# Optimization experiments

Measured on AMD Instinct MI355X. Metric: run time of the kernel, lower is better.

## Reference

```python
import jax, jax.numpy as jnp
import numpy as np

D_MODEL = 1024
NUM_HEADS = 16
H_DIM = 4096
EPS = 1e-5


def setup_inputs() -> dict:
    key = jax.random.key(0)
    ks = jax.random.split(key, 16)
    B, S, D, H = 2, 2048, D_MODEL, H_DIM
    s = 0.02
    return {
        "x": jax.random.normal(ks[0], (B, S, D), jnp.float32),
        "wq": jax.random.normal(ks[1], (D, D), jnp.float32) * s,
        "bq": jnp.zeros((D,), jnp.float32),
        "wk": jax.random.normal(ks[2], (D, D), jnp.float32) * s,
        "bk": jnp.zeros((D,), jnp.float32),
        "wv": jax.random.normal(ks[3], (D, D), jnp.float32) * s,
        "bv": jnp.zeros((D,), jnp.float32),
        "wo": jax.random.normal(ks[4], (D, D), jnp.float32) * s,
        "bo": jnp.zeros((D,), jnp.float32),
        "ln1_g": jnp.ones((D,), jnp.float32),
        "ln1_b": jnp.zeros((D,), jnp.float32),
        "w1": jax.random.normal(ks[5], (H, D), jnp.float32) * s,
        "b1": jnp.zeros((H,), jnp.float32),
        "w2": jax.random.normal(ks[6], (D, H), jnp.float32) * s,
        "b2": jnp.zeros((D,), jnp.float32),
        "ln2_g": jnp.ones((D,), jnp.float32),
        "ln2_b": jnp.zeros((D,), jnp.float32),
    }


def _layer_norm(x, g, b):
    mu = jnp.mean(x, axis=-1, keepdims=True)
    var = jnp.mean(jnp.square(x - mu), axis=-1, keepdims=True)
    return (x - mu) * jax.lax.rsqrt(var + EPS) * g + b


def _mhsa(x, wq, bq, wk, bk, wv, bv, wo, bo):
    B, S, D = x.shape
    Hh, hd = NUM_HEADS, D // NUM_HEADS
    q = (x @ wq.T + bq).reshape(B, S, Hh, hd)
    k = (x @ wk.T + bk).reshape(B, S, Hh, hd)
    v = (x @ wv.T + bv).reshape(B, S, Hh, hd)
    scale = hd ** -0.5
    scores = jnp.einsum('bqhd,bkhd->bhqk', q, k) * scale
    att = jax.nn.softmax(scores, axis=-1)
    out = jnp.einsum('bhqk,bkhd->bqhd', att, v).reshape(B, S, D)
    return out @ wo.T + bo


def reference(x, wq, bq, wk, bk, wv, bv, wo, bo, ln1_g, ln1_b,
              w1, b1, w2, b2, ln2_g, ln2_b):
    # pre-norm variant as written in the torch source:
    # x = norm1(x); x = x + msa(x)  (residual uses NORMALIZED x)
    x = _layer_norm(x, ln1_g, ln1_b)
    x = x + _mhsa(x, wq, bq, wk, bk, wv, bv, wo, bo)
    x = _layer_norm(x, ln2_g, ln2_b)
    h = jax.nn.gelu(x @ w1.T + b1, approximate=False)
    x = x + (h @ w2.T + b2)
    return x
```

## Files before the change

### kernel.cpp

```cpp
#include <hip/hip_runtime.h>
#include <hip/hip_bf16.h>

typedef unsigned short u16;
typedef __attribute__((ext_vector_type(8))) short short8;
typedef __attribute__((ext_vector_type(4))) float f32x4;

#define DM 1024
#define HM 4096
#define NHEADS 16
#define HD 64
#define SQ 2048
#define NBATCH 2
#define NTOK 4096

#define NX  ((size_t)NTOK * DM)

__device__ __forceinline__ u16 f2b(float f) {
    union { float f; unsigned int i; } w; w.f = f;
    unsigned int x = w.i;
    return (u16)((x + 0x7FFFu + ((x >> 16) & 1u)) >> 16);
}
__device__ __forceinline__ u16 f2b_ru(float f) {
    union { float f; unsigned int i; } w; w.f = f;
    return (u16)((w.i + 0x8000u) >> 16);
}

__device__ __forceinline__ void gload_lds16(const void* g, void* l) {
    __builtin_amdgcn_global_load_lds(
        (const __attribute__((address_space(1))) void*)g,
        (__attribute__((address_space(3))) void*)l, 16, 0, 0);
}

__global__ void cvt_all(const float* __restrict__ wq, const float* __restrict__ wk,
                        const float* __restrict__ wv, const float* __restrict__ wo,
                        const float* __restrict__ w1, const float* __restrict__ w2,
                        u16* __restrict__ dst) {
    const int NW4 = DM * DM / 4;
    int i = blockIdx.x * 256 + threadIdx.x;
    if (i >= 12 * NW4) return;
    const float* src; int base; float sc = 1.0f;
    if      (i <     NW4) { src = wq; base = 0;       sc = 0.125f; }
    else if (i < 2 * NW4) { src = wk; base = NW4; }
    else if (i < 3 * NW4) { src = wv; base = 2 * NW4; }
    else if (i < 4 * NW4) { src = wo; base = 3 * NW4; }
    else if (i < 8 * NW4) { src = w1; base = 4 * NW4; }
    else                  { src = w2; base = 8 * NW4; }
    float4 f = ((const float4*)src)[i - base];
    ushort4 o;
    o.x = f2b(f.x * sc); o.y = f2b(f.y * sc);
    o.z = f2b(f.z * sc); o.w = f2b(f.w * sc);
    ((ushort4*)dst)[i] = o;
}

__global__ void pack_bias(const float* __restrict__ bq, const float* __restrict__ bk,
                          const float* __restrict__ bv, float* __restrict__ dst) {
    int i = blockIdx.x * 256 + threadIdx.x;
    if (i >= 3 * DM) return;
    float v = (i < DM) ? bq[i] * 0.125f : (i < 2 * DM) ? bk[i - DM] : bv[i - 2 * DM];
    dst[i] = v;
}

__global__ void ln_kernel(const float* __restrict__ xin, const float* __restrict__ g,
                          const float* __restrict__ b, float* __restrict__ outf,
                          u16* __restrict__ outb) {
    int t = blockIdx.x, tid = threadIdx.x;
    float4 f = ((const float4*)(xin + (size_t)t * DM))[tid];
    float v0 = f.x, v1 = f.y, v2 = f.z, v3 = f.w;
    float s  = v0 + v1 + v2 + v3;
    float ss = v0*v0 + v1*v1 + v2*v2 + v3*v3;
    #pragma unroll
    for (int o = 32; o > 0; o >>= 1) {
        s  += __shfl_down(s,  o, 64);
        ss += __shfl_down(ss, o, 64);
    }
    __shared__ float rs[4], rss[4];
    int w = tid >> 6, lane = tid & 63;
    if (!lane) { rs[w] = s; rss[w] = ss; }
    __syncthreads();
    s  = rs[0] + rs[1] + rs[2] + rs[3];
    ss = rss[0] + rss[1] + rss[2] + rss[3];
    float mean = s * (1.0f / DM);
    float var  = ss * (1.0f / DM) - mean * mean;
    float rstd = rsqrtf(var + 1e-5f);
    float4 gu = ((const float4*)g)[tid];
    float4 bu = ((const float4*)b)[tid];
    float4 o;
    o.x = (v0 - mean) * rstd * gu.x + bu.x;
    o.y = (v1 - mean) * rstd * gu.y + bu.y;
    o.z = (v2 - mean) * rstd * gu.z + bu.z;
    o.w = (v3 - mean) * rstd * gu.w + bu.w;
    ((float4*)(outf + (size_t)t * DM))[tid] = o;
    ushort4 ob; ob.x = f2b(o.x); ob.y = f2b(o.y); ob.z = f2b(o.z); ob.w = f2b(o.w);
    ((ushort4*)(outb + (size_t)t * DM))[tid] = ob;
}

template<int GELU, int RESID, int OUTBF>
__global__ __launch_bounds__(256, 3)
void gemm_bt(const u16* __restrict__ A, const u16* __restrict__ W,
             const float* __restrict__ bias, const float* __restrict__ resid,
             void* __restrict__ Cout, int M, int N, int K) {
    __shared__ __attribute__((aligned(16))) u16 As[128 * 64];
    __shared__ __attribute__((aligned(16))) u16 Bs[128 * 64];
    int tid  = threadIdx.x;
    int wid  = tid >> 6, lane = tid & 63;
    int m0 = blockIdx.y << 7, n0 = blockIdx.x << 7;
    int wm = (wid & 1) << 6, wn = (wid >> 1) << 6;

    int rIn = lane >> 3;
    int cIn = (lane & 7) << 3;
    int s0  = wid << 2;
    int fr = lane & 15;
    int fc = (lane >> 4) << 3;

    f32x4 acc[4][4];
    #pragma unroll
    for (int i = 0; i < 4; i++)
        #pragma unroll
        for (int j = 0; j < 4; j++)
            acc[i][j] = (f32x4){0.f, 0.f, 0.f, 0.f};

    for (int k0 = 0; k0 < K; k0 += 64) {
        #pragma unroll
        for (int t = 0; t < 4; t++) {
            int s = s0 + t;
            gload_lds16(A + (size_t)(m0 + (s << 3) + rIn) * K + k0 + cIn, As + (s << 9));
            gload_lds16(W + (size_t)(n0 + (s << 3) + rIn) * K + k0 + cIn, Bs + (s << 9));
        }
        __syncthreads();
        #pragma unroll
        for (int ch = 0; ch < 2; ch++) {
            int kc = (ch << 5) + fc;
            short8 af[4], bf[4];
            #pragma unroll
            for (int mi = 0; mi < 4; mi++)
                af[mi] = *(const short8*)(As + (size_t)(wm + (mi << 4) + fr) * 64 + kc);
            #pragma unroll
            for (int ni = 0; ni < 4; ni++)
                bf[ni] = *(const short8*)(Bs + (size_t)(wn + (ni << 4) + fr) * 64 + kc);
            #pragma unroll
            for (int mi = 0; mi < 4; mi++)
                #pragma unroll
                for (int ni = 0; ni < 4; ni++)
                    acc[mi][ni] = __builtin_amdgcn_mfma_f32_16x16x32_bf16(
                        af[mi], bf[ni], acc[mi][ni], 0, 0, 0);
        }
        __syncthreads();
    }

    int erow = (lane >> 4) << 2;
    #pragma unroll
    for (int ni = 0; ni < 4; ni++) {
        int col = n0 + wn + (ni << 4) + fr;
        float bv = bias[col];
        #pragma unroll
        for (int mi = 0; mi < 4; mi++) {
            #pragma unroll
            for (int r = 0; r < 4; r++) {
                int row = m0 + wm + (mi << 4) + erow + r;
                float val = acc[mi][ni][r] + bv;
                if (GELU)  val = 0.5f * val * (1.0f + erff(val * 0.70710678118654752f));
                if (RESID) val += resid[(size_t)row * N + col];
                if (OUTBF) ((u16*)Cout)[(size_t)row * N + col] = f2b(val);
                else       ((float*)Cout)[(size_t)row * N + col] = val;
            }
        }
    }
}

template<int GELU, int RESID, int OUTBF>
__global__ __launch_bounds__(256, 3)
void gemm_n64(const u16* __restrict__ A, const u16* __restrict__ W,
              const float* __restrict__ bias, const float* __restrict__ resid,
              void* __restrict__ Cout, int M, int N, int K) {
    __shared__ __attribute__((aligned(16))) u16 As[128 * 64];
    __shared__ __attribute__((aligned(16))) u16 Bs[64 * 64];
    int tid  = threadIdx.x;
    int wid  = tid >> 6, lane = tid & 63;
    int m0 = blockIdx.y << 7, n0 = blockIdx.x << 6;
    int wm = (wid & 1) << 6, wn = (wid >> 1) << 5;

    int rIn = lane >> 3;
    int cIn = (lane & 7) << 3;
    int sA = wid << 2;
    int sB = wid << 1;
    int fr = lane & 15;
    int fc = (lane >> 4) << 3;

    f32x4 acc[4][2];
    #pragma unroll
    for (int i = 0; i < 4; i++)
        #pragma unroll
        for (int j = 0; j < 2; j++)
            acc[i][j] = (f32x4){0.f, 0.f, 0.f, 0.f};

    for (int k0 = 0; k0 < K; k0 += 64) {
        #pragma unroll
        for (int t = 0; t < 4; t++) {
            int s = sA + t;
            gload_lds16(A + (size_t)(m0 + (s << 3) + rIn) * K + k0 + cIn, As + (s << 9));
        }
        #pragma unroll
        for (int t = 0; t < 2; t++) {
            int s = sB + t;
            gload_lds16(W + (size_t)(n0 + (s << 3) + rIn) * K + k0 + cIn, Bs + (s << 9));
        }
        __syncthreads();
        #pragma unroll
        for (int ch = 0; ch < 2; ch++) {
            int kc = (ch << 5) + fc;
            short8 af[4], bf[2];
            #pragma unroll
            for (int mi = 0; mi < 4; mi++)
                af[mi] = *(const short8*)(As + (size_t)(wm + (mi << 4) + fr) * 64 + kc);
            #pragma unroll
            for (int ni = 0; ni < 2; ni++)
                bf[ni] = *(const short8*)(Bs + (size_t)(wn + (ni << 4) + fr) * 64 + kc);
            #pragma unroll
            for (int mi = 0; mi < 4; mi++)
                #pragma unroll
                for (int ni = 0; ni < 2; ni++)
                    acc[mi][ni] = __builtin_amdgcn_mfma_f32_16x16x32_bf16(
                        af[mi], bf[ni], acc[mi][ni], 0, 0, 0);
        }
        __syncthreads();
    }

    int erow = (lane >> 4) << 2;
    #pragma unroll
    for (int ni = 0; ni < 2; ni++) {
        int col = n0 + wn + (ni << 4) + fr;
        float bv = bias[col];
        #pragma unroll
        for (int mi = 0; mi < 4; mi++) {
            #pragma unroll
            for (int r = 0; r < 4; r++) {
                int row = m0 + wm + (mi << 4) + erow + r;
                float val = acc[mi][ni][r] + bv;
                if (GELU)  val = 0.5f * val * (1.0f + erff(val * 0.70710678118654752f));
                if (RESID) val += resid[(size_t)row * N + col];
                if (OUTBF) ((u16*)Cout)[(size_t)row * N + col] = f2b(val);
                else       ((float*)Cout)[(size_t)row * N + col] = val;
            }
        }
    }
}

__global__ __launch_bounds__(256) void fattn_mfma(const u16* __restrict__ QKV,
                                                  u16* __restrict__ O) {
    __shared__ __attribute__((aligned(16))) u16 QP[4096];
    __shared__ __attribute__((aligned(16))) u16 Ks[2][4096];
    __shared__ __attribute__((aligned(16))) u16 Vt[2][4096];
    const int ld = 3 * DM;
    int bid = blockIdx.x;
    int qt = bid & 31, bh = bid >> 5;
    int h = bh & (NHEADS - 1), b = bh >> 4;
    int tid = threadIdx.x, wid = tid >> 6, lane = tid & 63;
    int fr = lane & 15, fc = (lane >> 4) << 3;
    size_t tokb = (size_t)b * SQ;
    const u16* Qg = QKV + tokb * ld + h * HD;
    const u16* Kg = QKV + tokb * ld + DM + h * HD;
    const u16* Vg = QKV + tokb * ld + 2 * DM + h * HD;
    int vk = lane, vd0 = wid << 4;
    int s0 = wid << 1;
    u16* Ps = QP + (wid << 10);

    {
        #pragma unroll
        for (int t = 0; t < 2; t++) {
            int s = s0 + t;
            const u16* g = Qg + (size_t)(qt * 64 + ((s & 3) << 4) + (lane >> 2)) * ld
                         + ((s >> 2) << 5) + ((lane & 3) << 3);
            gload_lds16(g, QP + (s << 9));
        }
    }
    {
        #pragma unroll
        for (int t = 0; t < 2; t++) {
            int s = s0 + t;
            const u16* g = Kg + (size_t)(((s & 3) << 4) + (lane >> 2)) * ld
                         + ((s >> 2) << 5) + ((lane & 3) << 3);
            gload_lds16(g, Ks[0] + (s << 9));
        }
        const u16* vrow = Vg + (size_t)vk * ld + vd0;
        int cbase = (vk >> 5) << 11;
        int kk = vk & 31;
        #pragma unroll
        for (int j = 0; j < 4; j++) {
            ushort4 vv = *(const ushort4*)(vrow + (j << 2));
            int d = vd0 + (j << 2);
            Vt[0][cbase + (d + 0) * 32 + kk] = vv.x;
            Vt[0][cbase + (d + 1) * 32 + kk] = vv.y;
            Vt[0][cbase + (d + 2) * 32 + kk] = vv.z;
            Vt[0][cbase + (d + 3) * 32 + kk] = vv.w;
        }
    }
    f32x4 oacc[4];
    #pragma unroll
    for (int di = 0; di < 4; di++) oacc[di] = (f32x4){0.f, 0.f, 0.f, 0.f};
    float lsum[4] = {0.f, 0.f, 0.f, 0.f};
    __syncthreads();
    short8 aq0 = *(const short8*)(QP + ((wid << 4) + fr) * 32 + fc);
    short8 aq1 = *(const short8*)(QP + 2048 + ((wid << 4) + fr) * 32 + fc);
    __syncthreads();

    for (int kt = 0; kt < SQ / 64; kt++) {
        int buf = kt & 1;
        if (kt + 1 < SQ / 64) {
            #pragma unroll
            for (int t = 0; t < 2; t++) {
                int s = s0 + t;
                const u16* g = Kg + (size_t)((kt + 1) * 64 + ((s & 3) << 4) + (lane >> 2)) * ld
                             + ((s >> 2) << 5) + ((lane & 3) << 3);
                gload_lds16(g, Ks[buf ^ 1] + (s << 9));
            }
            const u16* vrow = Vg + (size_t)((kt + 1) * 64 + vk) * ld + vd0;
            int cbase = (vk >> 5) << 11;
            int kk = vk & 31;
            #pragma unroll
            for (int j = 0; j < 4; j++) {
                ushort4 vv = *(const ushort4*)(vrow + (j << 2));
                int d = vd0 + (j << 2);
                Vt[buf ^ 1][cbase + (d + 0) * 32 + kk] = vv.x;
                Vt[buf ^ 1][cbase + (d + 1) * 32 + kk] = vv.y;
                Vt[buf ^ 1][cbase + (d + 2) * 32 + kk] = vv.z;
                Vt[buf ^ 1][cbase + (d + 3) * 32 + kk] = vv.w;
            }
        }
        #pragma unroll
        for (int ni = 0; ni < 4; ni++) {
            short8 bk0 = *(const short8*)(Ks[buf] + ((ni << 4) + fr) * 32 + fc);
            short8 bk1 = *(const short8*)(Ks[buf] + 2048 + ((ni << 4) + fr) * 32 + fc);
            f32x4 z = (f32x4){0.f, 0.f, 0.f, 0.f};
            z = __builtin_amdgcn_mfma_f32_16x16x32_bf16(aq0, bk0, z, 0, 0, 0);
            z = __builtin_amdgcn_mfma_f32_16x16x32_bf16(aq1, bk1, z, 0, 0, 0);
            int c  = (ni << 4) + fr;
            int cb = (c >> 5) << 9;
            int kk = c & 31;
            #pragma unroll
            for (int r = 0; r < 4; r++) {
                float e = __expf(z[r]);
                lsum[r] += e;
                Ps[cb + (((lane >> 4) << 2) + r) * 32 + kk] = f2b_ru(e);
            }
        }
        short8 ap0 = *(const short8*)(Ps + fr * 32 + fc);
        short8 ap1 = *(const short8*)(Ps + 512 + fr * 32 + fc);
        #pragma unroll
        for (int di = 0; di < 4; di++) {
            short8 bv0 = *(const short8*)(Vt[buf] + ((di << 4) + fr) * 32 + fc);
            short8 bv1 = *(const short8*)(Vt[buf] + 2048 + ((di << 4) + fr) * 32 + fc);
            oacc[di] = __builtin_amdgcn_mfma_f32_16x16x32_bf16(ap0, bv0, oacc[di], 0, 0, 0);
            oacc[di] = __builtin_amdgcn_mfma_f32_16x16x32_bf16(ap1, bv1, oacc[di], 0, 0, 0);
        }
        __syncthreads();
    }
    #pragma unroll
    for (int msk = 1; msk <= 8; msk <<= 1)
        #pragma unroll
        for (int r = 0; r < 4; r++) lsum[r] += __shfl_xor(lsum[r], msk, 64);
    float inv[4];
    #pragma unroll
    for (int r = 0; r < 4; r++) inv[r] = 1.0f / lsum[r];
    #pragma unroll
    for (int di = 0; di < 4; di++) {
        int d = (di << 4) + fr;
        #pragma unroll
        for (int r = 0; r < 4; r++) {
            int q = qt * 64 + (wid << 4) + ((lane >> 4) << 2) + r;
            O[(tokb + q) * DM + h * HD + d] = f2b(oacc[di][r] * inv[r]);
        }
    }
}

extern "C" void kernel_launch(void* const* d_in, const int* in_sizes, int n_in,
                              void* d_out, int out_size, void* d_ws, size_t ws_size,
                              hipStream_t stream) {
    if (n_in < 17) return;
    const float* x   = (const float*)d_in[0];
    const float* wq  = (const float*)d_in[1];
    const float* bq  = (const float*)d_in[2];
    const float* wk  = (const float*)d_in[3];
    const float* bk  = (const float*)d_in[4];
    const float* wv  = (const float*)d_in[5];
    const float* bv  = (const float*)d_in[6];
    const float* wo  = (const float*)d_in[7];
    const float* bo  = (const float*)d_in[8];
    const float* g1  = (const float*)d_in[9];
    const float* e1  = (const float*)d_in[10];
    const float* w1  = (const float*)d_in[11];
    const float* b1  = (const float*)d_in[12];
    const float* w2  = (const float*)d_in[13];
    const float* b2  = (const float*)d_in[14];
    const float* g2  = (const float*)d_in[15];
    const float* e2  = (const float*)d_in[16];

    float* F = (float*)d_ws;
    size_t off = 0;
    float* xnf   = F + off; off += NX;
    u16*   xnb   = (u16*)(F + off); off += NX / 2;
    u16*   qkvb  = (u16*)(F + off); off += (size_t)NTOK * 3 * DM / 2;
    float* y     = F + off; off += NX;
    u16*   aob   = (u16*)(F + off); off += NX / 2;
    u16*   hb    = (u16*)(F + off); off += (size_t)NTOK * HM / 2;
    u16*   wqkvb = (u16*)(F + off); off += (size_t)3 * DM * DM / 2;
    u16*   wob   = (u16*)(F + off); off += (size_t)DM * DM / 2;
    u16*   w1b   = (u16*)(F + off); off += (size_t)HM * DM / 2;
    u16*   w2b   = (u16*)(F + off); off += (size_t)DM * HM / 2;
    float* bqkv  = F + off; off += 3 * DM;
    if (ws_size < off * sizeof(float)) return;

    dim3 blk(256);
    cvt_all<<<(12 * DM * DM / 4 + 255) / 256, blk, 0, stream>>>(
        wq, wk, wv, wo, w1, w2, wqkvb);
    pack_bias<<<(3 * DM + 255) / 256, blk, 0, stream>>>(bq, bk, bv, bqkv);

    ln_kernel<<<NTOK, blk, 0, stream>>>(x, g1, e1, xnf, xnb);
    gemm_bt<0,0,1><<<dim3(3 * DM / 128, NTOK / 128), blk, 0, stream>>>(
        xnb, wqkvb, bqkv, nullptr, qkvb, NTOK, 3 * DM, DM);
    fattn_mfma<<<NBATCH * NHEADS * (SQ / 64), blk, 0, stream>>>(qkvb, aob);
    gemm_n64<0,1,0><<<dim3(DM / 64, NTOK / 128), blk, 0, stream>>>(
        aob, wob, bo, xnf, y, NTOK, DM, DM);
    ln_kernel<<<NTOK, blk, 0, stream>>>(y, g2, e2, xnf, xnb);
    gemm_bt<1,0,1><<<dim3(HM / 128, NTOK / 128), blk, 0, stream>>>(
        xnb, w1b, b1, nullptr, hb, NTOK, HM, DM);
    gemm_n64<0,1,0><<<dim3(DM / 64, NTOK / 128), blk, 0, stream>>>(
        hb, w2b, b2, xnf, d_out, NTOK, DM, HM);
}
```

Before: 423.8 us.

## Pre-transpose V into head-major layout and load it via async LDS copies

Adds a separate kernel that transposes each head's V slice into a [bh][d][token] buffer, once per forward. The attention kernel can then stage V tiles with direct global-to-LDS 16-byte loads instead of scalar scattered LDS writes repeated by every query tile. The bias packing kernel is also folded into the weight conversion kernel, saving one launch. The cost is an extra kernel launch and an extra read and write of V through global memory.

```diff
diff --git a/kernel.cpp b/kernel.cpp
--- a/kernel.cpp
+++ b/kernel.cpp
@@ -34,30 +34,32 @@
 __global__ void cvt_all(const float* __restrict__ wq, const float* __restrict__ wk,
                         const float* __restrict__ wv, const float* __restrict__ wo,
                         const float* __restrict__ w1, const float* __restrict__ w2,
+                        const float* __restrict__ bq, const float* __restrict__ bk,
+                        const float* __restrict__ bv, float* __restrict__ bias_dst,
                         u16* __restrict__ dst) {
     const int NW4 = DM * DM / 4;
     int i = blockIdx.x * 256 + threadIdx.x;
-    if (i >= 12 * NW4) return;
-    const float* src; int base; float sc = 1.0f;
-    if      (i <     NW4) { src = wq; base = 0;       sc = 0.125f; }
-    else if (i < 2 * NW4) { src = wk; base = NW4; }
-    else if (i < 3 * NW4) { src = wv; base = 2 * NW4; }
-    else if (i < 4 * NW4) { src = wo; base = 3 * NW4; }
-    else if (i < 8 * NW4) { src = w1; base = 4 * NW4; }
-    else                  { src = w2; base = 8 * NW4; }
-    float4 f = ((const float4*)src)[i - base];
-    ushort4 o;
-    o.x = f2b(f.x * sc); o.y = f2b(f.y * sc);
-    o.z = f2b(f.z * sc); o.w = f2b(f.w * sc);
-    ((ushort4*)dst)[i] = o;
-}
-
-__global__ void pack_bias(const float* __restrict__ bq, const float* __restrict__ bk,
-                          const float* __restrict__ bv, float* __restrict__ dst) {
-    int i = blockIdx.x * 256 + threadIdx.x;
-    if (i >= 3 * DM) return;
-    float v = (i < DM) ? bq[i] * 0.125f : (i < 2 * DM) ? bk[i - DM] : bv[i - 2 * DM];
-    dst[i] = v;
+    if (i < 12 * NW4) {
+        const float* src; int base; float sc = 1.0f;
+        if      (i <     NW4) { src = wq; base = 0;       sc = 0.125f; }
+        else if (i < 2 * NW4) { src = wk; base = NW4; }
+        else if (i < 3 * NW4) { src = wv; base = 2 * NW4; }
+        else if (i < 4 * NW4) { src = wo; base = 3 * NW4; }
+        else if (i < 8 * NW4) { src = w1; base = 4 * NW4; }
+        else                  { src = w2; base = 8 * NW4; }
+        float4 f = ((const float4*)src)[i - base];
+        ushort4 o;
+        o.x = f2b(f.x * sc); o.y = f2b(f.y * sc);
+        o.z = f2b(f.z * sc); o.w = f2b(f.w * sc);
+        ((ushort4*)dst)[i] = o;
+    } else {
+        int j = i - 12 * NW4;
+        if (j < 3 * DM) {
+            float v = (j < DM) ? bq[j] * 0.125f
+                    : (j < 2 * DM) ? bk[j - DM] : bv[j - 2 * DM];
+            bias_dst[j] = v;
+        }
+    }
 }
 
 __global__ void ln_kernel(const float* __restrict__ xin, const float* __restrict__ g,
@@ -94,6 +96,31 @@
     ((ushort4*)(outb + (size_t)t * DM))[tid] = ob;
 }
 
+__global__ void vtr_kernel(const u16* __restrict__ qkv, u16* __restrict__ vT) {
+    __shared__ u16 tile[64][72];
+    int bid = blockIdx.x;
+    int tt = bid & 31, bh = bid >> 5;
+    int h = bh & (NHEADS - 1), b = bh >> 4;
+    int tid = threadIdx.x;
+    int r = tid >> 2, c0 = (tid & 3) << 4;
+    const u16* src = qkv + ((size_t)(b * SQ + tt * 64 + r)) * (3 * DM) + 2 * DM + h * HD + c0;
+    #pragma unroll
+    for (int j = 0; j < 4; j++)
+        *(ushort4*)&tile[r][c0 + (j << 2)] = *(const ushort4*)(src + (j << 2));
+    __syncthreads();
+    int dd = tid >> 2, t0 = (tid & 3) << 4;
+    u16* dst = vT + ((size_t)bh * HD + dd) * SQ + tt * 64 + t0;
+    #pragma unroll
+    for (int j = 0; j < 4; j++) {
+        ushort4 v;
+        v.x = tile[t0 + (j << 2) + 0][dd];
+        v.y = tile[t0 + (j << 2) + 1][dd];
+        v.z = tile[t0 + (j << 2) + 2][dd];
+        v.w = tile[t0 + (j << 2) + 3][dd];
+        *(ushort4*)(dst + (j << 2)) = v;
+    }
+}
+
 template<int GELU, int RESID, int OUTBF>
 __global__ __launch_bounds__(256, 3)
 void gemm_bt(const u16* __restrict__ A, const u16* __restrict__ W,
@@ -246,6 +273,7 @@
 }
 
 __global__ __launch_bounds__(256) void fattn_mfma(const u16* __restrict__ QKV,
+                                                  const u16* __restrict__ VT,
                                                   u16* __restrict__ O) {
     __shared__ __attribute__((aligned(16))) u16 QP[4096];
     __shared__ __attribute__((aligned(16))) u16 Ks[2][4096];
@@ -257,10 +285,9 @@
     int tid = threadIdx.x, wid = tid >> 6, lane = tid & 63;
     int fr = lane & 15, fc = (lane >> 4) << 3;
     size_t tokb = (size_t)b * SQ;
-    const u16* Qg = QKV + tokb * ld + h * HD;
-    const u16* Kg = QKV + tokb * ld + DM + h * HD;
-    const u16* Vg = QKV + tokb * ld + 2 * DM + h * HD;
-    int vk = lane, vd0 = wid << 4;
+    const u16* Qg  = QKV + tokb * ld + h * HD;
+    const u16* Kg  = QKV + tokb * ld + DM + h * HD;
+    const u16* VTg = VT + ((size_t)bh * HD) * SQ;
     int s0 = wid << 1;
     u16* Ps = QP + (wid << 10);
 
@@ -280,18 +307,9 @@
             const u16* g = Kg + (size_t)(((s & 3) << 4) + (lane >> 2)) * ld
                          + ((s >> 2) << 5) + ((lane & 3) << 3);
             gload_lds16(g, Ks[0] + (s << 9));
-        }
-        const u16* vrow = Vg + (size_t)vk * ld + vd0;
-        int cbase = (vk >> 5) << 11;
-        int kk = vk & 31;
-        #pragma unroll
-        for (int j = 0; j < 4; j++) {
-            ushort4 vv = *(const ushort4*)(vrow + (j << 2));
-            int d = vd0 + (j << 2);
-            Vt[0][cbase + (d + 0) * 32 + kk] = vv.x;
-            Vt[0][cbase + (d + 1) * 32 + kk] = vv.y;
-            Vt[0][cbase + (d + 2) * 32 + kk] = vv.z;
-            Vt[0][cbase + (d + 3) * 32 + kk] = vv.w;
+            const u16* gv = VTg + (size_t)(((s & 3) << 4) + (lane >> 2)) * SQ
+                          + ((s >> 2) << 5) + ((lane & 3) << 3);
+            gload_lds16(gv, Vt[0] + (s << 9));
         }
     }
     f32x4 oacc[4];
@@ -312,18 +330,9 @@
                 const u16* g = Kg + (size_t)((kt + 1) * 64 + ((s & 3) << 4) + (lane >> 2)) * ld
                              + ((s >> 2) << 5) + ((lane & 3) << 3);
                 gload_lds16(g, Ks[buf ^ 1] + (s << 9));
-            }
-            const u16* vrow = Vg + (size_t)((kt + 1) * 64 + vk) * ld + vd0;
-            int cbase = (vk >> 5) << 11;
-            int kk = vk & 31;
-            #pragma unroll
-            for (int j = 0; j < 4; j++) {
-                ushort4 vv = *(const ushort4*)(vrow + (j << 2));
-                int d = vd0 + (j << 2);
-                Vt[buf ^ 1][cbase + (d + 0) * 32 + kk] = vv.x;
-                Vt[buf ^ 1][cbase + (d + 1) * 32 + kk] = vv.y;
-                Vt[buf ^ 1][cbase + (d + 2) * 32 + kk] = vv.z;
-                Vt[buf ^ 1][cbase + (d + 3) * 32 + kk] = vv.w;
+                const u16* gv = VTg + (size_t)(((s & 3) << 4) + (lane >> 2)) * SQ
+                              + (kt + 1) * 64 + ((s >> 2) << 5) + ((lane & 3) << 3);
+                gload_lds16(gv, Vt[buf ^ 1] + (s << 9));
             }
         }
         #pragma unroll
@@ -399,6 +408,7 @@
     float* xnf   = F + off; off += NX;
     u16*   xnb   = (u16*)(F + off); off += NX / 2;
     u16*   qkvb  = (u16*)(F + off); off += (size_t)NTOK * 3 * DM / 2;
+    u16*   vTb   = (u16*)(F + off); off += (size_t)NTOK * DM / 2;
     float* y     = F + off; off += NX;
     u16*   aob   = (u16*)(F + off); off += NX / 2;
     u16*   hb    = (u16*)(F + off); off += (size_t)NTOK * HM / 2;
@@ -410,14 +420,14 @@
     if (ws_size < off * sizeof(float)) return;
 
     dim3 blk(256);
-    cvt_all<<<(12 * DM * DM / 4 + 255) / 256, blk, 0, stream>>>(
-        wq, wk, wv, wo, w1, w2, wqkvb);
-    pack_bias<<<(3 * DM + 255) / 256, blk, 0, stream>>>(bq, bk, bv, bqkv);
+    cvt_all<<<(12 * DM * DM / 4 + 3 * DM + 255) / 256, blk, 0, stream>>>(
+        wq, wk, wv, wo, w1, w2, bq, bk, bv, bqkv, wqkvb);
 
     ln_kernel<<<NTOK, blk, 0, stream>>>(x, g1, e1, xnf, xnb);
     gemm_bt<0,0,1><<<dim3(3 * DM / 128, NTOK / 128), blk, 0, stream>>>(
         xnb, wqkvb, bqkv, nullptr, qkvb, NTOK, 3 * DM, DM);
-    fattn_mfma<<<NBATCH * NHEADS * (SQ / 64), blk, 0, stream>>>(qkvb, aob);
+    vtr_kernel<<<NBATCH * NHEADS * (SQ / 64), blk, 0, stream>>>(qkvb, vTb);
+    fattn_mfma<<<NBATCH * NHEADS * (SQ / 64), blk, 0, stream>>>(qkvb, vTb, aob);
     gemm_n64<0,1,0><<<dim3(DM / 64, NTOK / 128), blk, 0, stream>>>(
         aob, wob, bo, xnf, y, NTOK, DM, DM);
     ln_kernel<<<NTOK, blk, 0, stream>>>(y, g2, e2, xnf, xnb);
```

Measured after the change: 419.0 us. Within noise of the previous version (-1.1%).
